# Optimization experiments

Hardware: AMD Instinct MI355X
Metric: run time of the kernel (lower is better)

The kernel has to match this reference:

```python
import jax, jax.numpy as jnp
import numpy as np

B, L, HID = 128, 256, 768
HID2 = 2 * HID
CDIM, SDIM, NPROJ = 192, 128, 128
FDIM = CDIM + SDIM + 1
BIG = 1e9  # finite pad so sorted invalid tokens go last without inf/nan issues


def setup_inputs() -> dict:
    key = jax.random.key(0)
    ks = jax.random.split(key, 12)
    H = jax.random.normal(ks[0], (B, L, HID), dtype=jnp.float32)
    tt = jax.random.randint(ks[1], (B, L), 0, 2, dtype=jnp.int32)
    m = jnp.ones((B, L), dtype=jnp.int32)
    s = 1.0 / np.sqrt(HID2)
    Wc = jax.random.uniform(ks[2], (CDIM, HID2), minval=-s, maxval=s, dtype=jnp.float32)
    bc = jax.random.uniform(ks[3], (CDIM,), minval=-s, maxval=s, dtype=jnp.float32)
    Ws = jax.random.uniform(ks[4], (SDIM, HID2), minval=-s, maxval=s, dtype=jnp.float32)
    bs = jax.random.uniform(ks[5], (SDIM,), minval=-s, maxval=s, dtype=jnp.float32)
    gate = jnp.array([0.5], dtype=jnp.float32)
    ln_g = jnp.ones((FDIM,), dtype=jnp.float32)
    ln_b = jnp.zeros((FDIM,), dtype=jnp.float32)
    sc = 1.0 / np.sqrt(FDIM)
    Wcls = jax.random.uniform(ks[6], (2, FDIM), minval=-sc, maxval=sc, dtype=jnp.float32)
    bcls = jax.random.uniform(ks[7], (2,), minval=-sc, maxval=sc, dtype=jnp.float32)
    d = jax.random.normal(ks[8], (NPROJ, HID), dtype=jnp.float32)
    proj_dirs = d / jnp.linalg.norm(d, axis=1, keepdims=True)
    return {"H": H, "tt": tt, "m": m, "Wc": Wc, "bc": bc, "Ws": Ws, "bs": bs,
            "gate": gate, "ln_g": ln_g, "ln_b": ln_b, "Wcls": Wcls, "bcls": bcls,
            "proj_dirs": proj_dirs}


def _forward(H, tt, m, Wc, bc, Ws, bs, gate, ln_g, ln_b, Wcls, bcls, proj_dirs):
    mask0 = (tt == 0) & (m == 1)  # [B,L]
    mask1 = (tt == 1) & (m == 1)
    f0 = mask0.astype(H.dtype)
    f1 = mask1.astype(H.dtype)
    cls = H[:, 0]  # [B,HID]
    mean0 = jnp.einsum('blh,bl->bh', H, f0) / jnp.clip(f0.sum(1, keepdims=True), 1.0)
    mean1 = jnp.einsum('blh,bl->bh', H, f1) / jnp.clip(f1.sum(1, keepdims=True), 1.0)
    rep = jnp.concatenate([cls, mean0 - mean1], axis=1)  # [B,2*HID]
    C = rep @ Wc.T + bc
    S = rep @ Ws.T + bs
    g = jax.nn.sigmoid(gate)  # [1]
    fused = jnp.concatenate([C * (1.0 - g), S * g], axis=1)

    # max-sliced W1 between token-type-0 and token-type-1 token sets, batched.
    P = jnp.einsum('blh,ph->blp', H, proj_dirs)  # [B,L,NPROJ]
    x0 = jnp.sort(jnp.where(mask0[..., None], P, BIG), axis=1)  # valid tokens first
    x1 = jnp.sort(jnp.where(mask1[..., None], P, BIG), axis=1)
    n0 = mask0.sum(1)
    n1 = mask1.sum(1)
    mcnt = jnp.minimum(n0, n1)  # [B]
    rmask = (jnp.arange(L)[None, :] < mcnt[:, None])[..., None]  # [B,L,1]
    diff = jnp.where(rmask, x0, 0.0) - jnp.where(rmask, x1, 0.0)
    mean_abs = jnp.abs(diff).sum(1) / jnp.maximum(mcnt, 1)[:, None].astype(P.dtype)  # [B,NPROJ]
    d_ot = mean_abs.max(axis=1, keepdims=True)  # [B,1]

    feat = jnp.concatenate([fused, d_ot], axis=1)  # [B,FDIM]
    mu = feat.mean(-1, keepdims=True)
    var = feat.var(-1, keepdims=True)
    normed = (feat - mu) * jax.lax.rsqrt(var + 1e-5) * ln_g + ln_b
    return normed @ Wcls.T + bcls  # [B,2]


def reference(H, tt, m, Wc, bc, Ws, bs, gate, ln_g, ln_b, Wcls, bcls, proj_dirs):
    return _forward(H, tt, m, Wc, bc, Ws, bs, gate, ln_g, ln_b, Wcls, bcls, proj_dirs)
```

## Files before the change

### kernel.cpp

```cpp
#include <hip/hip_runtime.h>
#include <cmath>

#define B_   128
#define L_   256
#define HID_ 768
#define HID2_ 1536
#define CDIM_ 192
#define SDIM_ 128
#define NPROJ_ 128
#define FDIM_ 321

typedef __attribute__((ext_vector_type(8))) short bf16x8;
typedef __attribute__((ext_vector_type(4))) float f32x4;

__device__ inline unsigned short bf_hi_trunc(float x) {
    return (unsigned short)(__float_as_uint(x) >> 16);
}
__device__ inline float bf2f(unsigned short s) {
    return __uint_as_float(((unsigned int)s) << 16);
}
__device__ inline unsigned short f2bf_rne(float x) {
    unsigned int u = __float_as_uint(x);
    unsigned int r = (u + 0x7fff + ((u >> 16) & 1)) >> 16;
    return (unsigned short)r;
}

__global__ __launch_bounds__(192) void pre_kernel(
    const float* __restrict__ Pd, unsigned short* __restrict__ Pjh,
    unsigned short* __restrict__ Pjl)
{
    int i = blockIdx.x * 192 + threadIdx.x;
    float4 v = ((const float4*)Pd)[i];
    ushort4 h, l;
    h.x = bf_hi_trunc(v.x); l.x = f2bf_rne(v.x - bf2f(h.x));
    h.y = bf_hi_trunc(v.y); l.y = f2bf_rne(v.y - bf2f(h.y));
    h.z = bf_hi_trunc(v.z); l.z = f2bf_rne(v.z - bf2f(h.z));
    h.w = bf_hi_trunc(v.w); l.w = f2bf_rne(v.w - bf2f(h.w));
    ((ushort4*)Pjh)[i] = h;
    ((ushort4*)Pjl)[i] = l;
}

__device__ inline void stats_add(float4 x, float4 y,
                                 float f0a, float f0b, float f1a, float f1b,
                                 int colbase, int lane, float (*sacc)[HID_])
{
    float p0x = x.x * f0a + y.x * f0b, p0y = x.y * f0a + y.y * f0b;
    float p0z = x.z * f0a + y.z * f0b, p0w = x.w * f0a + y.w * f0b;
    float p1x = x.x * f1a + y.x * f1b, p1y = x.y * f1a + y.y * f1b;
    float p1z = x.z * f1a + y.z * f1b, p1w = x.w * f1a + y.w * f1b;
#pragma unroll
    for (int off = 8; off < 64; off <<= 1) {
        p0x += __shfl_xor(p0x, off, 64); p0y += __shfl_xor(p0y, off, 64);
        p0z += __shfl_xor(p0z, off, 64); p0w += __shfl_xor(p0w, off, 64);
        p1x += __shfl_xor(p1x, off, 64); p1y += __shfl_xor(p1y, off, 64);
        p1z += __shfl_xor(p1z, off, 64); p1w += __shfl_xor(p1w, off, 64);
    }
    if (lane < 8) {
        float* d0 = &sacc[0][colbase + lane * 4];
        float* d1 = &sacc[1][colbase + lane * 4];
        atomicAdd(d0 + 0, p0x); atomicAdd(d0 + 1, p0y);
        atomicAdd(d0 + 2, p0z); atomicAdd(d0 + 3, p0w);
        atomicAdd(d1 + 0, p1x); atomicAdd(d1 + 1, p1y);
        atomicAdd(d1 + 2, p1z); atomicAdd(d1 + 3, p1w);
    }
}

#define LDSROW 72
__global__ __launch_bounds__(256, 3) void gemm_mfma(
    const float* __restrict__ H, const unsigned short* __restrict__ Pjh,
    const unsigned short* __restrict__ Pjl, const int* __restrict__ tt,
    const int* __restrict__ mm, float* __restrict__ Pt,
    float* __restrict__ part)
{
    __shared__ unsigned short Hs[2][64 * LDSROW];
    __shared__ float sf0[64], sf1[64];
    __shared__ float sacc[2][HID_];

    int tid = threadIdx.x;
    int w = tid >> 6;
    int lane = tid & 63;
    int c = lane & 15;
    int q = lane >> 4;

    int b = blockIdx.x >> 2;
    int lbase = (blockIdx.x & 3) * 64;

    const float* Hbase = H + ((size_t)(b * L_ + lbase)) * HID_;

    int hrow0 = tid >> 3;
    int hc4   = tid & 7;

    if (tid < 64) {
        int t  = tt[b * L_ + lbase + tid];
        int mv = mm[b * L_ + lbase + tid];
        sf0[tid] = (t == 0 && mv == 1) ? 1.f : 0.f;
        sf1[tid] = (t == 1 && mv == 1) ? 1.f : 0.f;
    }
    for (int i = tid; i < 2 * HID_; i += 256)
        (&sacc[0][0])[i] = 0.f;

    const unsigned short* pjh0 = Pjh + (size_t)(w * 32 + c) * HID_ + q * 8;
    const unsigned short* pjh1 = Pjh + (size_t)(w * 32 + 16 + c) * HID_ + q * 8;
    const unsigned short* pjl0 = Pjl + (size_t)(w * 32 + c) * HID_ + q * 8;
    const unsigned short* pjl1 = Pjl + (size_t)(w * 32 + 16 + c) * HID_ + q * 8;

    f32x4 acc[2][4] = {};

    float4 hreg[2];
    uint4 cah[2], cal[2];
    uint4 nah[2], nal[2];

    hreg[0] = *(const float4*)(Hbase + (size_t)hrow0 * HID_ + hc4 * 4);
    hreg[1] = *(const float4*)(Hbase + (size_t)(hrow0 + 32) * HID_ + hc4 * 4);
    cah[0] = *(const uint4*)(pjh0);
    cah[1] = *(const uint4*)(pjh1);
    cal[0] = *(const uint4*)(pjl0);
    cal[1] = *(const uint4*)(pjl1);
#pragma unroll
    for (int u = 0; u < 2; ++u) {
        int row = hrow0 + u * 32;
        float4 v = hreg[u];
        ushort4 h, l;
        h.x = bf_hi_trunc(v.x); l.x = f2bf_rne(v.x - bf2f(h.x));
        h.y = bf_hi_trunc(v.y); l.y = f2bf_rne(v.y - bf2f(h.y));
        h.z = bf_hi_trunc(v.z); l.z = f2bf_rne(v.z - bf2f(h.z));
        h.w = bf_hi_trunc(v.w); l.w = f2bf_rne(v.w - bf2f(h.w));
        *(ushort4*)&Hs[0][row * LDSROW + hc4 * 4]      = h;
        *(ushort4*)&Hs[0][row * LDSROW + 32 + hc4 * 4] = l;
    }
    __syncthreads();

    float f0a = sf0[hrow0], f0b = sf0[hrow0 + 32];
    float f1a = sf1[hrow0], f1b = sf1[hrow0 + 32];

    stats_add(hreg[0], hreg[1], f0a, f0b, f1a, f1b, 0, lane, sacc);

    for (int it = 0; it < 24; ++it) {
        int cur = it & 1;
        int nxt = cur ^ 1;

        if (it + 1 < 24) {
            int k0 = (it + 1) * 32;
            hreg[0] = *(const float4*)(Hbase + (size_t)hrow0 * HID_ + k0 + hc4 * 4);
            hreg[1] = *(const float4*)(Hbase + (size_t)(hrow0 + 32) * HID_ + k0 + hc4 * 4);
            nah[0] = *(const uint4*)(pjh0 + k0);
            nah[1] = *(const uint4*)(pjh1 + k0);
            nal[0] = *(const uint4*)(pjl0 + k0);
            nal[1] = *(const uint4*)(pjl1 + k0);
        }

        bf16x8 bh[4], bl[4];
#pragma unroll
        for (int lt = 0; lt < 4; ++lt) {
            int l = lt * 16 + c;
            bh[lt] = *(const bf16x8*)&Hs[cur][l * LDSROW + q * 8];
            bl[lt] = *(const bf16x8*)&Hs[cur][l * LDSROW + 32 + q * 8];
        }
        bf16x8 ah[2], al[2];
        ah[0] = *(bf16x8*)&cah[0]; ah[1] = *(bf16x8*)&cah[1];
        al[0] = *(bf16x8*)&cal[0]; al[1] = *(bf16x8*)&cal[1];

#pragma unroll
        for (int pt = 0; pt < 2; ++pt)
#pragma unroll
        for (int lt = 0; lt < 4; ++lt) {
            acc[pt][lt] = __builtin_amdgcn_mfma_f32_16x16x32_bf16(ah[pt], bh[lt], acc[pt][lt], 0, 0, 0);
            acc[pt][lt] = __builtin_amdgcn_mfma_f32_16x16x32_bf16(ah[pt], bl[lt], acc[pt][lt], 0, 0, 0);
            acc[pt][lt] = __builtin_amdgcn_mfma_f32_16x16x32_bf16(al[pt], bh[lt], acc[pt][lt], 0, 0, 0);
        }

        if (it + 1 < 24) {
#pragma unroll
            for (int u = 0; u < 2; ++u) {
                int row = hrow0 + u * 32;
                float4 v = hreg[u];
                ushort4 h, l;
                h.x = bf_hi_trunc(v.x); l.x = f2bf_rne(v.x - bf2f(h.x));
                h.y = bf_hi_trunc(v.y); l.y = f2bf_rne(v.y - bf2f(h.y));
                h.z = bf_hi_trunc(v.z); l.z = f2bf_rne(v.z - bf2f(h.z));
                h.w = bf_hi_trunc(v.w); l.w = f2bf_rne(v.w - bf2f(h.w));
                *(ushort4*)&Hs[nxt][row * LDSROW + hc4 * 4]      = h;
                *(ushort4*)&Hs[nxt][row * LDSROW + 32 + hc4 * 4] = l;
            }
            stats_add(hreg[0], hreg[1], f0a, f0b, f1a, f1b,
                      (it + 1) * 32, lane, sacc);
            cah[0] = nah[0]; cah[1] = nah[1];
            cal[0] = nal[0]; cal[1] = nal[1];
        }
        __syncthreads();
    }

#pragma unroll
    for (int pt = 0; pt < 2; ++pt)
#pragma unroll
    for (int lt = 0; lt < 4; ++lt)
#pragma unroll
    for (int r = 0; r < 4; ++r) {
        int p = w * 32 + pt * 16 + q * 4 + r;
        int l = lbase + lt * 16 + c;
        Pt[((size_t)(b * NPROJ_ + p)) * L_ + l] = acc[pt][lt][r];
    }

    {
        float* pdst = part + (size_t)(b * 4 + (blockIdx.x & 3)) * HID2_;
        for (int i = tid; i < HID2_; i += 256)
            pdst[i] = (&sacc[0][0])[i];
    }
}

__global__ __launch_bounds__(256) void headot_kernel(
    const float* __restrict__ H, const int* __restrict__ tt,
    const int* __restrict__ mm, const float* __restrict__ part,
    const float* __restrict__ Wc, const float* __restrict__ bc,
    const float* __restrict__ Ws, const float* __restrict__ bs,
    const float* __restrict__ gate, const float* __restrict__ Pt,
    float* __restrict__ fused, float* __restrict__ dist)
{
    if (blockIdx.x < B_ * 8) {
        __shared__ float srep[HID2_];
        int b = blockIdx.x >> 3;
        int ochunk = (blockIdx.x & 7) * 40;
        int tid = threadIdx.x;

        int t  = tt[b * L_ + tid];
        int mv = mm[b * L_ + tid];
        int n0 = __syncthreads_count(t == 0 && mv == 1);
        int n1 = __syncthreads_count(t == 1 && mv == 1);
        float r0 = 1.f / fmaxf((float)n0, 1.f);
        float r1 = 1.f / fmaxf((float)n1, 1.f);

        const float* pp = part + (size_t)b * 4 * HID2_;
        for (int h = tid; h < HID_; h += 256) {
            float a0 = pp[h] + pp[HID2_ + h] + pp[2 * HID2_ + h] + pp[3 * HID2_ + h];
            float a1 = pp[HID_ + h] + pp[HID2_ + HID_ + h]
                     + pp[2 * HID2_ + HID_ + h] + pp[3 * HID2_ + HID_ + h];
            srep[h]        = H[(size_t)b * L_ * HID_ + h];
            srep[HID_ + h] = a0 * r0 - a1 * r1;
        }
        __syncthreads();

        int w = tid >> 6;
        int lane = tid & 63;
        float g = 1.0f / (1.0f + expf(-gate[0]));

#pragma unroll
        for (int r = 0; r < 10; ++r) {
            int o = ochunk + r * 4 + w;
            bool isC = (o < CDIM_);
            const float4* wr = (const float4*)(isC ? (Wc + (size_t)o * HID2_)
                                                   : (Ws + (size_t)(o - CDIM_) * HID2_));
            float acc = 0.f;
#pragma unroll
            for (int u = 0; u < 6; ++u) {
                int k4 = lane + u * 64;
                float4 a = *(const float4*)&srep[k4 * 4];
                float4 ww = wr[k4];
                acc += a.x * ww.x + a.y * ww.y + a.z * ww.z + a.w * ww.w;
            }
            for (int off = 32; off; off >>= 1) acc += __shfl_xor(acc, off, 64);
            if (lane == 0) {
                float bias = isC ? bc[o] : bs[o - CDIM_];
                float scale = isC ? (1.0f - g) : g;
                fused[(size_t)b * (CDIM_ + SDIM_) + o] = (acc + bias) * scale;
            }
        }
        return;
    }

    int bid = blockIdx.x - B_ * 8;
    int w = bid * 4 + (threadIdx.x >> 6);
    int lane = threadIdx.x & 63;
    int b = w >> 7;
    int p = w & (NPROJ_ - 1);

    float4 pv = *(const float4*)(Pt + ((size_t)(b * NPROJ_ + p)) * L_ + lane * 4);
    int4 t4 = *(const int4*)(tt + (size_t)b * L_ + lane * 4);
    int4 m4 = *(const int4*)(mm + (size_t)b * L_ + lane * 4);

    float pvals[4] = {pv.x, pv.y, pv.z, pv.w};
    int tv[4] = {t4.x, t4.y, t4.z, t4.w};
    int mv[4] = {m4.x, m4.y, m4.z, m4.w};

    unsigned key[4];
#pragma unroll
    for (int r = 0; r < 4; ++r) {
        unsigned u = __float_as_uint(pvals[r]);
        unsigned s = (u & 0x80000000u) ? ~u : (u | 0x80000000u);
        unsigned label = (mv[r] == 1) ? (unsigned)tv[r] : 2u;
        key[r] = (s & ~3u) | label;
    }

    {
        unsigned mn0 = min(key[0], key[1]), mx0 = max(key[0], key[1]);
        key[0] = mn0; key[1] = mx0;
        unsigned mn1 = min(key[2], key[3]), mx1 = max(key[2], key[3]);
        key[2] = mx1; key[3] = mn1;
    }
#pragma unroll
    for (int k = 4; k <= 256; k <<= 1) {
        bool up = (lane & (k >> 2)) == 0;
#pragma unroll
        for (int j = k >> 1; j >= 4; j >>= 1) {
            int lj = j >> 2;
#pragma unroll
            for (int r = 0; r < 4; ++r) {
                unsigned o = (unsigned)__shfl_xor((int)key[r], lj, 64);
                bool lower = (lane & lj) == 0;
                unsigned mn = min(key[r], o), mx = max(key[r], o);
                key[r] = (lower == up) ? mn : mx;
            }
        }
        {
            unsigned mn0 = min(key[0], key[2]), mx0 = max(key[0], key[2]);
            key[0] = up ? mn0 : mx0; key[2] = up ? mx0 : mn0;
            unsigned mn1 = min(key[1], key[3]), mx1 = max(key[1], key[3]);
            key[1] = up ? mn1 : mx1; key[3] = up ? mx1 : mn1;
        }
        {
            unsigned mn0 = min(key[0], key[1]), mx0 = max(key[0], key[1]);
            key[0] = up ? mn0 : mx0; key[1] = up ? mx0 : mn0;
            unsigned mn1 = min(key[2], key[3]), mx1 = max(key[2], key[3]);
            key[2] = up ? mn1 : mx1; key[3] = up ? mx1 : mn1;
        }
    }

    int lab[4];
    float tval[4];
    unsigned sincl[4];
    unsigned run = 0;
#pragma unroll
    for (int r = 0; r < 4; ++r) {
        lab[r] = (int)(key[r] & 3u);
        unsigned s = key[r] & ~3u;
        unsigned u = (s & 0x80000000u) ? (s ^ 0x80000000u) : ~s;
        tval[r] = __uint_as_float(u);
        unsigned unit = ((lab[r] == 0) ? 0x10000u : 0u) | ((lab[r] == 1) ? 1u : 0u);
        run += unit;
        sincl[r] = run;
    }
    unsigned inc = run;
#pragma unroll
    for (int d = 1; d < 64; d <<= 1) {
        unsigned tt2 = (unsigned)__shfl_up((int)inc, d, 64);
        if (lane >= d) inc += tt2;
    }
    unsigned ex = inc - run;
    unsigned total = (unsigned)__shfl((int)inc, 63, 64);
    int n0 = (int)(total >> 16), n1 = (int)(total & 0xffffu);
    int m = (n0 < n1) ? n0 : n1;

    float ssum = 0.f;
#pragma unroll
    for (int r = 0; r < 4; ++r) {
        unsigned C = ex + sincl[r];
        int c0 = (int)(C >> 16), c1 = (int)(C & 0xffffu);
        int s0 = (lab[r] == 0), s1 = (lab[r] == 1);
        int wi = abs(min(c0, m) - min(c1, m));
        int wp = abs(min(c0 - s0, m) - min(c1 - s1, m));
        ssum += tval[r] * (float)(wp - wi);
    }
    for (int off = 32; off; off >>= 1) ssum += __shfl_xor(ssum, off, 64);
    if (lane == 0) dist[b * NPROJ_ + p] = ssum / (float)((m > 1) ? m : 1);
}

__global__ __launch_bounds__(64) void final_kernel(
    const float* __restrict__ fused, const float* __restrict__ dist,
    const float* __restrict__ ln_g, const float* __restrict__ ln_b,
    const float* __restrict__ Wcls, const float* __restrict__ bcls,
    float* __restrict__ out)
{
    int b = blockIdx.x;
    int lane = threadIdx.x;

    float mx = fmaxf(dist[b * NPROJ_ + lane], dist[b * NPROJ_ + 64 + lane]);
    for (int off = 32; off; off >>= 1) mx = fmaxf(mx, __shfl_xor(mx, off, 64));

    float fv[6];
    float sum = 0.f, sq = 0.f;
#pragma unroll
    for (int u = 0; u < 6; ++u) {
        int j = lane + u * 64;
        float x = 0.f;
        if (j < CDIM_ + SDIM_) x = fused[(size_t)b * (CDIM_ + SDIM_) + j];
        else if (j == CDIM_ + SDIM_) x = mx;
        fv[u] = x;
        if (j < FDIM_) { sum += x; sq += x * x; }
    }
    for (int off = 32; off; off >>= 1) {
        sum += __shfl_xor(sum, off, 64);
        sq  += __shfl_xor(sq,  off, 64);
    }
    float mu = sum / (float)FDIM_;
    float var = sq / (float)FDIM_ - mu * mu;
    float inv = rsqrtf(var + 1e-5f);

    float d0 = 0.f, d1 = 0.f;
#pragma unroll
    for (int u = 0; u < 6; ++u) {
        int j = lane + u * 64;
        if (j < FDIM_) {
            float nx = (fv[u] - mu) * inv * ln_g[j] + ln_b[j];
            d0 += nx * Wcls[j];
            d1 += nx * Wcls[FDIM_ + j];
        }
    }
    for (int off = 32; off; off >>= 1) {
        d0 += __shfl_xor(d0, off, 64);
        d1 += __shfl_xor(d1, off, 64);
    }
    if (lane == 0) {
        out[b * 2 + 0] = d0 + bcls[0];
        out[b * 2 + 1] = d1 + bcls[1];
    }
}

extern "C" void kernel_launch(void* const* d_in, const int* in_sizes, int n_in,
                              void* d_out, int out_size, void* d_ws, size_t ws_size,
                              hipStream_t stream)
{
    const float* H    = (const float*)d_in[0];
    const int*   tt   = (const int*)d_in[1];
    const int*   mm   = (const int*)d_in[2];
    const float* Wc   = (const float*)d_in[3];
    const float* bc   = (const float*)d_in[4];
    const float* Ws   = (const float*)d_in[5];
    const float* bs   = (const float*)d_in[6];
    const float* gate = (const float*)d_in[7];
    const float* ln_g = (const float*)d_in[8];
    const float* ln_b = (const float*)d_in[9];
    const float* Wcls = (const float*)d_in[10];
    const float* bcls = (const float*)d_in[11];
    const float* Pd   = (const float*)d_in[12];
    float* out = (float*)d_out;

    float* ws = (float*)d_ws;
    float* Pt    = ws;
    float* part  = Pt + (size_t)B_ * NPROJ_ * L_;
    float* rep   = part + (size_t)B_ * 8 * HID2_;
    float* fused = rep + (size_t)B_ * HID2_;
    float* dist  = fused + (size_t)B_ * (CDIM_ + SDIM_);
    unsigned short* Pjh = (unsigned short*)(dist + (size_t)B_ * NPROJ_);
    unsigned short* Pjl = Pjh + (size_t)NPROJ_ * HID_;

    pre_kernel<<<128, 192, 0, stream>>>(Pd, Pjh, Pjl);
    gemm_mfma<<<B_ * 4, 256, 0, stream>>>(H, Pjh, Pjl, tt, mm, Pt, part);
    headot_kernel<<<B_ * 8 + B_ * NPROJ_ / 4, 256, 0, stream>>>(
        H, tt, mm, part, Wc, bc, Ws, bs, gate, Pt, fused, dist);
    final_kernel<<<B_, 64, 0, stream>>>(fused, dist, ln_g, ln_b, Wcls, bcls, out);
}
```

Measured before the change: 230.8 us.

## Split projection GEMM into 32-token blocks and fold mask weights into stats

The projection GEMM now runs 8 blocks per batch row with 32 tokens each instead of 4 blocks with 64, and raises the occupancy hint from 3 to 4 blocks per SM. The two masked mean accumulators become one signed weighted sum: each token's weight is +1/n0, -1/n1 or 0, and counts are computed inside the GEMM kernel. Stats use per-element LDS atomics in place of the shuffle reduction, and the main loop is unrolled by two with ping-pong registers. The intent is more parallelism, less LDS and fewer stat operations, at the cost of reloading the projection weights twice as often and heavier atomic contention on LDS.

```diff
diff --git a/kernel.cpp b/kernel.cpp
--- a/kernel.cpp
+++ b/kernel.cpp
@@ -40,41 +40,17 @@
     ((ushort4*)Pjl)[i] = l;
 }
 
-__device__ inline void stats_add(float4 x, float4 y,
-                                 float f0a, float f0b, float f1a, float f1b,
-                                 int colbase, int lane, float (*sacc)[HID_])
-{
-    float p0x = x.x * f0a + y.x * f0b, p0y = x.y * f0a + y.y * f0b;
-    float p0z = x.z * f0a + y.z * f0b, p0w = x.w * f0a + y.w * f0b;
-    float p1x = x.x * f1a + y.x * f1b, p1y = x.y * f1a + y.y * f1b;
-    float p1z = x.z * f1a + y.z * f1b, p1w = x.w * f1a + y.w * f1b;
-#pragma unroll
-    for (int off = 8; off < 64; off <<= 1) {
-        p0x += __shfl_xor(p0x, off, 64); p0y += __shfl_xor(p0y, off, 64);
-        p0z += __shfl_xor(p0z, off, 64); p0w += __shfl_xor(p0w, off, 64);
-        p1x += __shfl_xor(p1x, off, 64); p1y += __shfl_xor(p1y, off, 64);
-        p1z += __shfl_xor(p1z, off, 64); p1w += __shfl_xor(p1w, off, 64);
-    }
-    if (lane < 8) {
-        float* d0 = &sacc[0][colbase + lane * 4];
-        float* d1 = &sacc[1][colbase + lane * 4];
-        atomicAdd(d0 + 0, p0x); atomicAdd(d0 + 1, p0y);
-        atomicAdd(d0 + 2, p0z); atomicAdd(d0 + 3, p0w);
-        atomicAdd(d1 + 0, p1x); atomicAdd(d1 + 1, p1y);
-        atomicAdd(d1 + 2, p1z); atomicAdd(d1 + 3, p1w);
-    }
-}
-
 #define LDSROW 72
-__global__ __launch_bounds__(256, 3) void gemm_mfma(
+#define LCH 32
+__global__ __launch_bounds__(256, 4) void gemm_mfma(
     const float* __restrict__ H, const unsigned short* __restrict__ Pjh,
     const unsigned short* __restrict__ Pjl, const int* __restrict__ tt,
     const int* __restrict__ mm, float* __restrict__ Pt,
     float* __restrict__ part)
 {
-    __shared__ unsigned short Hs[2][64 * LDSROW];
-    __shared__ float sf0[64], sf1[64];
-    __shared__ float sacc[2][HID_];
+    __shared__ unsigned short Hs[2][LCH * LDSROW];
+    __shared__ float sacc[HID_];
+    __shared__ float sw[LCH];
 
     int tid = threadIdx.x;
     int w = tid >> 6;
@@ -82,118 +58,111 @@
     int c = lane & 15;
     int q = lane >> 4;
 
-    int b = blockIdx.x >> 2;
-    int lbase = (blockIdx.x & 3) * 64;
+    int b = blockIdx.x >> 3;
+    int lbase = (blockIdx.x & 7) * LCH;
 
     const float* Hbase = H + ((size_t)(b * L_ + lbase)) * HID_;
-
-    int hrow0 = tid >> 3;
-    int hc4   = tid & 7;
-
-    if (tid < 64) {
-        int t  = tt[b * L_ + lbase + tid];
-        int mv = mm[b * L_ + lbase + tid];
-        sf0[tid] = (t == 0 && mv == 1) ? 1.f : 0.f;
-        sf1[tid] = (t == 1 && mv == 1) ? 1.f : 0.f;
-    }
-    for (int i = tid; i < 2 * HID_; i += 256)
-        (&sacc[0][0])[i] = 0.f;
+    int hrow = tid >> 3;
+    int hc4  = tid & 7;
 
     const unsigned short* pjh0 = Pjh + (size_t)(w * 32 + c) * HID_ + q * 8;
-    const unsigned short* pjh1 = Pjh + (size_t)(w * 32 + 16 + c) * HID_ + q * 8;
+    const unsigned short* pjh1 = pjh0 + (size_t)16 * HID_;
     const unsigned short* pjl0 = Pjl + (size_t)(w * 32 + c) * HID_ + q * 8;
-    const unsigned short* pjl1 = Pjl + (size_t)(w * 32 + 16 + c) * HID_ + q * 8;
-
-    f32x4 acc[2][4] = {};
-
-    float4 hreg[2];
-    uint4 cah[2], cal[2];
-    uint4 nah[2], nal[2];
-
-    hreg[0] = *(const float4*)(Hbase + (size_t)hrow0 * HID_ + hc4 * 4);
-    hreg[1] = *(const float4*)(Hbase + (size_t)(hrow0 + 32) * HID_ + hc4 * 4);
-    cah[0] = *(const uint4*)(pjh0);
-    cah[1] = *(const uint4*)(pjh1);
-    cal[0] = *(const uint4*)(pjl0);
-    cal[1] = *(const uint4*)(pjl1);
-#pragma unroll
-    for (int u = 0; u < 2; ++u) {
-        int row = hrow0 + u * 32;
-        float4 v = hreg[u];
-        ushort4 h, l;
-        h.x = bf_hi_trunc(v.x); l.x = f2bf_rne(v.x - bf2f(h.x));
-        h.y = bf_hi_trunc(v.y); l.y = f2bf_rne(v.y - bf2f(h.y));
-        h.z = bf_hi_trunc(v.z); l.z = f2bf_rne(v.z - bf2f(h.z));
-        h.w = bf_hi_trunc(v.w); l.w = f2bf_rne(v.w - bf2f(h.w));
-        *(ushort4*)&Hs[0][row * LDSROW + hc4 * 4]      = h;
-        *(ushort4*)&Hs[0][row * LDSROW + 32 + hc4 * 4] = l;
-    }
+    const unsigned short* pjl1 = pjl0 + (size_t)16 * HID_;
+
+    float4 hreg0, hreg1;
+    uint4 ah00, ah01, al00, al01;
+    uint4 ah10, ah11, al10, al11;
+    f32x4 acc[2][2] = {};
+
+#define LOADR(S, T) do {                                                      \
+    int k0_ = (T) * 32;                                                       \
+    hreg##S = *(const float4*)(Hbase + (size_t)hrow * HID_ + k0_ + hc4 * 4);  \
+    ah##S##0 = *(const uint4*)(pjh0 + k0_);                                   \
+    ah##S##1 = *(const uint4*)(pjh1 + k0_);                                   \
+    al##S##0 = *(const uint4*)(pjl0 + k0_);                                   \
+    al##S##1 = *(const uint4*)(pjl1 + k0_);                                   \
+} while (0)
+
+#define CONVSTAT(S, BUF, T) do {                                              \
+    float4 v_ = hreg##S;                                                      \
+    ushort4 h_, l_;                                                           \
+    h_.x = bf_hi_trunc(v_.x); l_.x = f2bf_rne(v_.x - bf2f(h_.x));             \
+    h_.y = bf_hi_trunc(v_.y); l_.y = f2bf_rne(v_.y - bf2f(h_.y));             \
+    h_.z = bf_hi_trunc(v_.z); l_.z = f2bf_rne(v_.z - bf2f(h_.z));             \
+    h_.w = bf_hi_trunc(v_.w); l_.w = f2bf_rne(v_.w - bf2f(h_.w));             \
+    *(ushort4*)&Hs[BUF][hrow * LDSROW + hc4 * 4]      = h_;                   \
+    *(ushort4*)&Hs[BUF][hrow * LDSROW + 32 + hc4 * 4] = l_;                   \
+    int cb_ = (T) * 32 + hc4 * 4;                                             \
+    atomicAdd(&sacc[cb_ + 0], v_.x * swt);                                    \
+    atomicAdd(&sacc[cb_ + 1], v_.y * swt);                                    \
+    atomicAdd(&sacc[cb_ + 2], v_.z * swt);                                    \
+    atomicAdd(&sacc[cb_ + 3], v_.w * swt);                                    \
+} while (0)
+
+#define GEMMSTEP(S, BUF) do {                                                 \
+    bf16x8 bh0_ = *(const bf16x8*)&Hs[BUF][(c)      * LDSROW + q * 8];        \
+    bf16x8 bh1_ = *(const bf16x8*)&Hs[BUF][(16 + c) * LDSROW + q * 8];        \
+    bf16x8 bl0_ = *(const bf16x8*)&Hs[BUF][(c)      * LDSROW + 32 + q * 8];   \
+    bf16x8 bl1_ = *(const bf16x8*)&Hs[BUF][(16 + c) * LDSROW + 32 + q * 8];   \
+    bf16x8 a0h_ = *(bf16x8*)&ah##S##0;                                        \
+    bf16x8 a1h_ = *(bf16x8*)&ah##S##1;                                        \
+    bf16x8 a0l_ = *(bf16x8*)&al##S##0;                                        \
+    bf16x8 a1l_ = *(bf16x8*)&al##S##1;                                        \
+    acc[0][0] = __builtin_amdgcn_mfma_f32_16x16x32_bf16(a0h_, bh0_, acc[0][0], 0, 0, 0); \
+    acc[0][1] = __builtin_amdgcn_mfma_f32_16x16x32_bf16(a0h_, bh1_, acc[0][1], 0, 0, 0); \
+    acc[1][0] = __builtin_amdgcn_mfma_f32_16x16x32_bf16(a1h_, bh0_, acc[1][0], 0, 0, 0); \
+    acc[1][1] = __builtin_amdgcn_mfma_f32_16x16x32_bf16(a1h_, bh1_, acc[1][1], 0, 0, 0); \
+    acc[0][0] = __builtin_amdgcn_mfma_f32_16x16x32_bf16(a0h_, bl0_, acc[0][0], 0, 0, 0); \
+    acc[0][1] = __builtin_amdgcn_mfma_f32_16x16x32_bf16(a0h_, bl1_, acc[0][1], 0, 0, 0); \
+    acc[1][0] = __builtin_amdgcn_mfma_f32_16x16x32_bf16(a1h_, bl0_, acc[1][0], 0, 0, 0); \
+    acc[1][1] = __builtin_amdgcn_mfma_f32_16x16x32_bf16(a1h_, bl1_, acc[1][1], 0, 0, 0); \
+    acc[0][0] = __builtin_amdgcn_mfma_f32_16x16x32_bf16(a0l_, bh0_, acc[0][0], 0, 0, 0); \
+    acc[0][1] = __builtin_amdgcn_mfma_f32_16x16x32_bf16(a0l_, bh1_, acc[0][1], 0, 0, 0); \
+    acc[1][0] = __builtin_amdgcn_mfma_f32_16x16x32_bf16(a1l_, bh0_, acc[1][0], 0, 0, 0); \
+    acc[1][1] = __builtin_amdgcn_mfma_f32_16x16x32_bf16(a1l_, bh1_, acc[1][1], 0, 0, 0); \
+} while (0)
+
+    LOADR(0, 0);
+    LOADR(1, 1);
+
+    int t_ = tt[b * L_ + tid];
+    int m_ = mm[b * L_ + tid];
+    int n0 = __syncthreads_count(t_ == 0 && m_ == 1);
+    int n1 = __syncthreads_count(t_ == 1 && m_ == 1);
+    float r0 = 1.f / fmaxf((float)n0, 1.f);
+    float r1 = 1.f / fmaxf((float)n1, 1.f);
+    if (tid < LCH) {
+        int tl = tt[b * L_ + lbase + tid];
+        int ml = mm[b * L_ + lbase + tid];
+        sw[tid] = ((tl == 0 && ml == 1) ? r0 : 0.f)
+                - ((tl == 1 && ml == 1) ? r1 : 0.f);
+    }
+    for (int i = tid; i < HID_; i += 256) sacc[i] = 0.f;
     __syncthreads();
-
-    float f0a = sf0[hrow0], f0b = sf0[hrow0 + 32];
-    float f1a = sf1[hrow0], f1b = sf1[hrow0 + 32];
-
-    stats_add(hreg[0], hreg[1], f0a, f0b, f1a, f1b, 0, lane, sacc);
-
-    for (int it = 0; it < 24; ++it) {
-        int cur = it & 1;
-        int nxt = cur ^ 1;
-
-        if (it + 1 < 24) {
-            int k0 = (it + 1) * 32;
-            hreg[0] = *(const float4*)(Hbase + (size_t)hrow0 * HID_ + k0 + hc4 * 4);
-            hreg[1] = *(const float4*)(Hbase + (size_t)(hrow0 + 32) * HID_ + k0 + hc4 * 4);
-            nah[0] = *(const uint4*)(pjh0 + k0);
-            nah[1] = *(const uint4*)(pjh1 + k0);
-            nal[0] = *(const uint4*)(pjl0 + k0);
-            nal[1] = *(const uint4*)(pjl1 + k0);
-        }
-
-        bf16x8 bh[4], bl[4];
-#pragma unroll
-        for (int lt = 0; lt < 4; ++lt) {
-            int l = lt * 16 + c;
-            bh[lt] = *(const bf16x8*)&Hs[cur][l * LDSROW + q * 8];
-            bl[lt] = *(const bf16x8*)&Hs[cur][l * LDSROW + 32 + q * 8];
-        }
-        bf16x8 ah[2], al[2];
-        ah[0] = *(bf16x8*)&cah[0]; ah[1] = *(bf16x8*)&cah[1];
-        al[0] = *(bf16x8*)&cal[0]; al[1] = *(bf16x8*)&cal[1];
-
-#pragma unroll
-        for (int pt = 0; pt < 2; ++pt)
-#pragma unroll
-        for (int lt = 0; lt < 4; ++lt) {
-            acc[pt][lt] = __builtin_amdgcn_mfma_f32_16x16x32_bf16(ah[pt], bh[lt], acc[pt][lt], 0, 0, 0);
-            acc[pt][lt] = __builtin_amdgcn_mfma_f32_16x16x32_bf16(ah[pt], bl[lt], acc[pt][lt], 0, 0, 0);
-            acc[pt][lt] = __builtin_amdgcn_mfma_f32_16x16x32_bf16(al[pt], bh[lt], acc[pt][lt], 0, 0, 0);
-        }
-
-        if (it + 1 < 24) {
-#pragma unroll
-            for (int u = 0; u < 2; ++u) {
-                int row = hrow0 + u * 32;
-                float4 v = hreg[u];
-                ushort4 h, l;
-                h.x = bf_hi_trunc(v.x); l.x = f2bf_rne(v.x - bf2f(h.x));
-                h.y = bf_hi_trunc(v.y); l.y = f2bf_rne(v.y - bf2f(h.y));
-                h.z = bf_hi_trunc(v.z); l.z = f2bf_rne(v.z - bf2f(h.z));
-                h.w = bf_hi_trunc(v.w); l.w = f2bf_rne(v.w - bf2f(h.w));
-                *(ushort4*)&Hs[nxt][row * LDSROW + hc4 * 4]      = h;
-                *(ushort4*)&Hs[nxt][row * LDSROW + 32 + hc4 * 4] = l;
-            }
-            stats_add(hreg[0], hreg[1], f0a, f0b, f1a, f1b,
-                      (it + 1) * 32, lane, sacc);
-            cah[0] = nah[0]; cah[1] = nah[1];
-            cal[0] = nal[0]; cal[1] = nal[1];
-        }
+    float swt = sw[hrow];
+
+    CONVSTAT(0, 0, 0);
+    __syncthreads();
+
+    for (int itp = 0; itp < 12; ++itp) {
+        int it0 = itp * 2;
+
+        GEMMSTEP(0, 0);
+        if (it0 + 2 < 24) LOADR(0, it0 + 2);
+        CONVSTAT(1, 1, it0 + 1);
         __syncthreads();
+
+        GEMMSTEP(1, 1);
+        if (it0 + 3 < 24) LOADR(1, it0 + 3);
+        if (it0 + 2 < 24) CONVSTAT(0, 0, it0 + 2);
+        __syncthreads();
     }
 
 #pragma unroll
     for (int pt = 0; pt < 2; ++pt)
 #pragma unroll
-    for (int lt = 0; lt < 4; ++lt)
+    for (int lt = 0; lt < 2; ++lt)
 #pragma unroll
     for (int r = 0; r < 4; ++r) {
         int p = w * 32 + pt * 16 + q * 4 + r;
@@ -202,10 +171,13 @@
     }
 
     {
-        float* pdst = part + (size_t)(b * 4 + (blockIdx.x & 3)) * HID2_;
-        for (int i = tid; i < HID2_; i += 256)
-            pdst[i] = (&sacc[0][0])[i];
-    }
+        float* pdst = part + (size_t)(b * 8 + (blockIdx.x & 7)) * HID_;
+        for (int i = tid; i < HID_; i += 256)
+            pdst[i] = sacc[i];
+    }
+#undef LOADR
+#undef CONVSTAT
+#undef GEMMSTEP
 }
 
 __global__ __launch_bounds__(256) void headot_kernel(
@@ -222,20 +194,13 @@
         int ochunk = (blockIdx.x & 7) * 40;
         int tid = threadIdx.x;
 
-        int t  = tt[b * L_ + tid];
-        int mv = mm[b * L_ + tid];
-        int n0 = __syncthreads_count(t == 0 && mv == 1);
-        int n1 = __syncthreads_count(t == 1 && mv == 1);
-        float r0 = 1.f / fmaxf((float)n0, 1.f);
-        float r1 = 1.f / fmaxf((float)n1, 1.f);
-
-        const float* pp = part + (size_t)b * 4 * HID2_;
+        const float* pp = part + (size_t)b * 8 * HID_;
         for (int h = tid; h < HID_; h += 256) {
-            float a0 = pp[h] + pp[HID2_ + h] + pp[2 * HID2_ + h] + pp[3 * HID2_ + h];
-            float a1 = pp[HID_ + h] + pp[HID2_ + HID_ + h]
-                     + pp[2 * HID2_ + HID_ + h] + pp[3 * HID2_ + HID_ + h];
+            float a = pp[h] + pp[HID_ + h] + pp[2 * HID_ + h] + pp[3 * HID_ + h]
+                    + pp[4 * HID_ + h] + pp[5 * HID_ + h] + pp[6 * HID_ + h]
+                    + pp[7 * HID_ + h];
             srep[h]        = H[(size_t)b * L_ * HID_ + h];
-            srep[HID_ + h] = a0 * r0 - a1 * r1;
+            srep[HID_ + h] = a;
         }
         __syncthreads();
 
@@ -443,7 +408,7 @@
     unsigned short* Pjl = Pjh + (size_t)NPROJ_ * HID_;
 
     pre_kernel<<<128, 192, 0, stream>>>(Pd, Pjh, Pjl);
-    gemm_mfma<<<B_ * 4, 256, 0, stream>>>(H, Pjh, Pjl, tt, mm, Pt, part);
+    gemm_mfma<<<B_ * 8, 256, 0, stream>>>(H, Pjh, Pjl, tt, mm, Pt, part);
     headot_kernel<<<B_ * 8 + B_ * NPROJ_ / 4, 256, 0, stream>>>(
         H, tt, mm, part, Wc, bc, Ws, bs, gate, Pt, fused, dist);
     final_kernel<<<B_, 64, 0, stream>>>(fused, dist, ln_g, ln_b, Wcls, bcls, out);
```

Measured after the change: 309.5 us. 34.1% more time.

## Split projection GEMM along K into two halves and fold mask weights into stats

Applied to the files above, without the earlier changes.

The projection GEMM grid now splits the hidden dimension into two halves, doubling the block count from 512 to 1024. Each half writes its own partial P buffer, and the sort/OT stage sums the two halves. The per-token-type stats are folded into a single signed, count-normalised weight, which halves the shuffle and atomic work and shrinks the partial buffers. This trades more parallelism and occupancy (launch bounds raised to 4) for an extra 16MB partial write and read of P.

```diff
diff --git a/kernel.cpp b/kernel.cpp
--- a/kernel.cpp
+++ b/kernel.cpp
@@ -9,6 +9,8 @@
 #define SDIM_ 128
 #define NPROJ_ 128
 #define FDIM_ 321
+#define KSL_ 384
+#define PTSTRIDE ((size_t)B_ * NPROJ_ * L_)
 
 typedef __attribute__((ext_vector_type(8))) short bf16x8;
 typedef __attribute__((ext_vector_type(4))) float f32x4;
@@ -40,41 +42,39 @@
     ((ushort4*)Pjl)[i] = l;
 }
 
-__device__ inline void stats_add(float4 x, float4 y,
-                                 float f0a, float f0b, float f1a, float f1b,
-                                 int colbase, int lane, float (*sacc)[HID_])
-{
-    float p0x = x.x * f0a + y.x * f0b, p0y = x.y * f0a + y.y * f0b;
-    float p0z = x.z * f0a + y.z * f0b, p0w = x.w * f0a + y.w * f0b;
-    float p1x = x.x * f1a + y.x * f1b, p1y = x.y * f1a + y.y * f1b;
-    float p1z = x.z * f1a + y.z * f1b, p1w = x.w * f1a + y.w * f1b;
+__device__ inline void stats_bfly(float4 x, float4 y, float fa, float fb,
+                                  int kbase, int lane, float* __restrict__ sacc)
+{
+    float px = x.x * fa + y.x * fb;
+    float py = x.y * fa + y.y * fb;
+    float pz = x.z * fa + y.z * fb;
+    float pw = x.w * fa + y.w * fb;
 #pragma unroll
     for (int off = 8; off < 64; off <<= 1) {
-        p0x += __shfl_xor(p0x, off, 64); p0y += __shfl_xor(p0y, off, 64);
-        p0z += __shfl_xor(p0z, off, 64); p0w += __shfl_xor(p0w, off, 64);
-        p1x += __shfl_xor(p1x, off, 64); p1y += __shfl_xor(p1y, off, 64);
-        p1z += __shfl_xor(p1z, off, 64); p1w += __shfl_xor(p1w, off, 64);
+        px += __shfl_xor(px, off, 64);
+        py += __shfl_xor(py, off, 64);
+        pz += __shfl_xor(pz, off, 64);
+        pw += __shfl_xor(pw, off, 64);
     }
     if (lane < 8) {
-        float* d0 = &sacc[0][colbase + lane * 4];
-        float* d1 = &sacc[1][colbase + lane * 4];
-        atomicAdd(d0 + 0, p0x); atomicAdd(d0 + 1, p0y);
-        atomicAdd(d0 + 2, p0z); atomicAdd(d0 + 3, p0w);
-        atomicAdd(d1 + 0, p1x); atomicAdd(d1 + 1, p1y);
-        atomicAdd(d1 + 2, p1z); atomicAdd(d1 + 3, p1w);
+        float* d = &sacc[kbase + lane * 4];
+        atomicAdd(d + 0, px);
+        atomicAdd(d + 1, py);
+        atomicAdd(d + 2, pz);
+        atomicAdd(d + 3, pw);
     }
 }
 
 #define LDSROW 72
-__global__ __launch_bounds__(256, 3) void gemm_mfma(
+__global__ __launch_bounds__(256, 4) void gemm_mfma(
     const float* __restrict__ H, const unsigned short* __restrict__ Pjh,
     const unsigned short* __restrict__ Pjl, const int* __restrict__ tt,
-    const int* __restrict__ mm, float* __restrict__ Pt,
+    const int* __restrict__ mm, float* __restrict__ Ptp,
     float* __restrict__ part)
 {
     __shared__ unsigned short Hs[2][64 * LDSROW];
-    __shared__ float sf0[64], sf1[64];
-    __shared__ float sacc[2][HID_];
+    __shared__ float sacc[KSL_];
+    __shared__ float sw[64];
 
     int tid = threadIdx.x;
     int w = tid >> 6;
@@ -82,30 +82,21 @@
     int c = lane & 15;
     int q = lane >> 4;
 
-    int b = blockIdx.x >> 2;
-    int lbase = (blockIdx.x & 3) * 64;
-
-    const float* Hbase = H + ((size_t)(b * L_ + lbase)) * HID_;
-
+    int ks     = blockIdx.x & 1;
+    int lchunk = (blockIdx.x >> 1) & 3;
+    int b      = blockIdx.x >> 3;
+    int lbase  = lchunk * 64;
+
+    const float* Hbase = H + ((size_t)(b * L_ + lbase)) * HID_ + ks * KSL_;
     int hrow0 = tid >> 3;
     int hc4   = tid & 7;
 
-    if (tid < 64) {
-        int t  = tt[b * L_ + lbase + tid];
-        int mv = mm[b * L_ + lbase + tid];
-        sf0[tid] = (t == 0 && mv == 1) ? 1.f : 0.f;
-        sf1[tid] = (t == 1 && mv == 1) ? 1.f : 0.f;
-    }
-    for (int i = tid; i < 2 * HID_; i += 256)
-        (&sacc[0][0])[i] = 0.f;
-
-    const unsigned short* pjh0 = Pjh + (size_t)(w * 32 + c) * HID_ + q * 8;
-    const unsigned short* pjh1 = Pjh + (size_t)(w * 32 + 16 + c) * HID_ + q * 8;
-    const unsigned short* pjl0 = Pjl + (size_t)(w * 32 + c) * HID_ + q * 8;
-    const unsigned short* pjl1 = Pjl + (size_t)(w * 32 + 16 + c) * HID_ + q * 8;
+    const unsigned short* pjh0 = Pjh + (size_t)(w * 32 + c) * HID_ + ks * KSL_ + q * 8;
+    const unsigned short* pjh1 = pjh0 + (size_t)16 * HID_;
+    const unsigned short* pjl0 = Pjl + (size_t)(w * 32 + c) * HID_ + ks * KSL_ + q * 8;
+    const unsigned short* pjl1 = pjl0 + (size_t)16 * HID_;
 
     f32x4 acc[2][4] = {};
-
     float4 hreg[2];
     uint4 cah[2], cal[2];
     uint4 nah[2], nal[2];
@@ -116,30 +107,45 @@
     cah[1] = *(const uint4*)(pjh1);
     cal[0] = *(const uint4*)(pjl0);
     cal[1] = *(const uint4*)(pjl1);
-#pragma unroll
-    for (int u = 0; u < 2; ++u) {
-        int row = hrow0 + u * 32;
-        float4 v = hreg[u];
-        ushort4 h, l;
-        h.x = bf_hi_trunc(v.x); l.x = f2bf_rne(v.x - bf2f(h.x));
-        h.y = bf_hi_trunc(v.y); l.y = f2bf_rne(v.y - bf2f(h.y));
-        h.z = bf_hi_trunc(v.z); l.z = f2bf_rne(v.z - bf2f(h.z));
-        h.w = bf_hi_trunc(v.w); l.w = f2bf_rne(v.w - bf2f(h.w));
-        *(ushort4*)&Hs[0][row * LDSROW + hc4 * 4]      = h;
-        *(ushort4*)&Hs[0][row * LDSROW + 32 + hc4 * 4] = l;
-    }
+
+    int t_ = tt[b * L_ + tid];
+    int m_ = mm[b * L_ + tid];
+    int n0 = __syncthreads_count(t_ == 0 && m_ == 1);
+    int n1 = __syncthreads_count(t_ == 1 && m_ == 1);
+    float r0 = 1.f / fmaxf((float)n0, 1.f);
+    float r1 = 1.f / fmaxf((float)n1, 1.f);
+    if (tid < 64) {
+        int tl = tt[b * L_ + lbase + tid];
+        int ml = mm[b * L_ + lbase + tid];
+        sw[tid] = ((tl == 0 && ml == 1) ? r0 : 0.f)
+                - ((tl == 1 && ml == 1) ? r1 : 0.f);
+    }
+    for (int i = tid; i < KSL_; i += 256) sacc[i] = 0.f;
     __syncthreads();
-
-    float f0a = sf0[hrow0], f0b = sf0[hrow0 + 32];
-    float f1a = sf1[hrow0], f1b = sf1[hrow0 + 32];
-
-    stats_add(hreg[0], hreg[1], f0a, f0b, f1a, f1b, 0, lane, sacc);
-
-    for (int it = 0; it < 24; ++it) {
+    float fa = sw[hrow0], fb = sw[hrow0 + 32];
+
+    {
+#pragma unroll
+        for (int u = 0; u < 2; ++u) {
+            int row = hrow0 + u * 32;
+            float4 v = hreg[u];
+            ushort4 h, l;
+            h.x = bf_hi_trunc(v.x); l.x = f2bf_rne(v.x - bf2f(h.x));
+            h.y = bf_hi_trunc(v.y); l.y = f2bf_rne(v.y - bf2f(h.y));
+            h.z = bf_hi_trunc(v.z); l.z = f2bf_rne(v.z - bf2f(h.z));
+            h.w = bf_hi_trunc(v.w); l.w = f2bf_rne(v.w - bf2f(h.w));
+            *(ushort4*)&Hs[0][row * LDSROW + hc4 * 4]      = h;
+            *(ushort4*)&Hs[0][row * LDSROW + 32 + hc4 * 4] = l;
+        }
+        stats_bfly(hreg[0], hreg[1], fa, fb, 0, lane, sacc);
+    }
+    __syncthreads();
+
+    for (int it = 0; it < 12; ++it) {
         int cur = it & 1;
         int nxt = cur ^ 1;
 
-        if (it + 1 < 24) {
+        if (it + 1 < 12) {
             int k0 = (it + 1) * 32;
             hreg[0] = *(const float4*)(Hbase + (size_t)hrow0 * HID_ + k0 + hc4 * 4);
             hreg[1] = *(const float4*)(Hbase + (size_t)(hrow0 + 32) * HID_ + k0 + hc4 * 4);
@@ -169,7 +175,7 @@
             acc[pt][lt] = __builtin_amdgcn_mfma_f32_16x16x32_bf16(al[pt], bh[lt], acc[pt][lt], 0, 0, 0);
         }
 
-        if (it + 1 < 24) {
+        if (it + 1 < 12) {
 #pragma unroll
             for (int u = 0; u < 2; ++u) {
                 int row = hrow0 + u * 32;
@@ -182,14 +188,14 @@
                 *(ushort4*)&Hs[nxt][row * LDSROW + hc4 * 4]      = h;
                 *(ushort4*)&Hs[nxt][row * LDSROW + 32 + hc4 * 4] = l;
             }
-            stats_add(hreg[0], hreg[1], f0a, f0b, f1a, f1b,
-                      (it + 1) * 32, lane, sacc);
+            stats_bfly(hreg[0], hreg[1], fa, fb, (it + 1) * 32, lane, sacc);
             cah[0] = nah[0]; cah[1] = nah[1];
             cal[0] = nal[0]; cal[1] = nal[1];
         }
         __syncthreads();
     }
 
+    float* Pts = Ptp + (size_t)ks * PTSTRIDE;
 #pragma unroll
     for (int pt = 0; pt < 2; ++pt)
 #pragma unroll
@@ -198,13 +204,13 @@
     for (int r = 0; r < 4; ++r) {
         int p = w * 32 + pt * 16 + q * 4 + r;
         int l = lbase + lt * 16 + c;
-        Pt[((size_t)(b * NPROJ_ + p)) * L_ + l] = acc[pt][lt][r];
+        Pts[((size_t)(b * NPROJ_ + p)) * L_ + l] = acc[pt][lt][r];
     }
 
     {
-        float* pdst = part + (size_t)(b * 4 + (blockIdx.x & 3)) * HID2_;
-        for (int i = tid; i < HID2_; i += 256)
-            pdst[i] = (&sacc[0][0])[i];
+        float* pdst = part + (size_t)(b * 4 + lchunk) * HID_ + ks * KSL_;
+        for (int i = tid; i < KSL_; i += 256)
+            pdst[i] = sacc[i];
     }
 }
 
@@ -213,7 +219,7 @@
     const int* __restrict__ mm, const float* __restrict__ part,
     const float* __restrict__ Wc, const float* __restrict__ bc,
     const float* __restrict__ Ws, const float* __restrict__ bs,
-    const float* __restrict__ gate, const float* __restrict__ Pt,
+    const float* __restrict__ gate, const float* __restrict__ Ptp,
     float* __restrict__ fused, float* __restrict__ dist)
 {
     if (blockIdx.x < B_ * 8) {
@@ -222,20 +228,11 @@
         int ochunk = (blockIdx.x & 7) * 40;
         int tid = threadIdx.x;
 
-        int t  = tt[b * L_ + tid];
-        int mv = mm[b * L_ + tid];
-        int n0 = __syncthreads_count(t == 0 && mv == 1);
-        int n1 = __syncthreads_count(t == 1 && mv == 1);
-        float r0 = 1.f / fmaxf((float)n0, 1.f);
-        float r1 = 1.f / fmaxf((float)n1, 1.f);
-
-        const float* pp = part + (size_t)b * 4 * HID2_;
+        const float* pp = part + (size_t)b * 4 * HID_;
         for (int h = tid; h < HID_; h += 256) {
-            float a0 = pp[h] + pp[HID2_ + h] + pp[2 * HID2_ + h] + pp[3 * HID2_ + h];
-            float a1 = pp[HID_ + h] + pp[HID2_ + HID_ + h]
-                     + pp[2 * HID2_ + HID_ + h] + pp[3 * HID2_ + HID_ + h];
+            float a = pp[h] + pp[HID_ + h] + pp[2 * HID_ + h] + pp[3 * HID_ + h];
             srep[h]        = H[(size_t)b * L_ * HID_ + h];
-            srep[HID_ + h] = a0 * r0 - a1 * r1;
+            srep[HID_ + h] = a;
         }
         __syncthreads();
 
@@ -273,7 +270,9 @@
     int b = w >> 7;
     int p = w & (NPROJ_ - 1);
 
-    float4 pv = *(const float4*)(Pt + ((size_t)(b * NPROJ_ + p)) * L_ + lane * 4);
+    float4 pv0 = *(const float4*)(Ptp + ((size_t)(b * NPROJ_ + p)) * L_ + lane * 4);
+    float4 pv1 = *(const float4*)(Ptp + PTSTRIDE + ((size_t)(b * NPROJ_ + p)) * L_ + lane * 4);
+    float4 pv = make_float4(pv0.x + pv1.x, pv0.y + pv1.y, pv0.z + pv1.z, pv0.w + pv1.w);
     int4 t4 = *(const int4*)(tt + (size_t)b * L_ + lane * 4);
     int4 m4 = *(const int4*)(mm + (size_t)b * L_ + lane * 4);
 
@@ -434,17 +433,16 @@
     float* out = (float*)d_out;
 
     float* ws = (float*)d_ws;
-    float* Pt    = ws;
-    float* part  = Pt + (size_t)B_ * NPROJ_ * L_;
-    float* rep   = part + (size_t)B_ * 8 * HID2_;
-    float* fused = rep + (size_t)B_ * HID2_;
+    float* Ptp   = ws;
+    float* part  = Ptp + 2 * PTSTRIDE;
+    float* fused = part + (size_t)B_ * 4 * HID_;
     float* dist  = fused + (size_t)B_ * (CDIM_ + SDIM_);
     unsigned short* Pjh = (unsigned short*)(dist + (size_t)B_ * NPROJ_);
     unsigned short* Pjl = Pjh + (size_t)NPROJ_ * HID_;
 
     pre_kernel<<<128, 192, 0, stream>>>(Pd, Pjh, Pjl);
-    gemm_mfma<<<B_ * 4, 256, 0, stream>>>(H, Pjh, Pjl, tt, mm, Pt, part);
+    gemm_mfma<<<B_ * 8, 256, 0, stream>>>(H, Pjh, Pjl, tt, mm, Ptp, part);
     headot_kernel<<<B_ * 8 + B_ * NPROJ_ / 4, 256, 0, stream>>>(
-        H, tt, mm, part, Wc, bc, Ws, bs, gate, Pt, fused, dist);
+        H, tt, mm, part, Wc, bc, Ws, bs, gate, Ptp, fused, dist);
     final_kernel<<<B_, 64, 0, stream>>>(fused, dist, ln_g, ln_b, Wcls, bcls, out);
 }
```

Result: faster. 224.2 us (-2.8%).
